# Kernel optimization log

Measured on AMD Instinct MI355X. Metric: run time of the kernel, lower is better.

Reference implementation:

```python
import jax, jax.numpy as jnp
import numpy as np


def setup_inputs() -> dict:
    key = jax.random.key(0)
    ks = jax.random.split(key, 7)
    d, nq, nk = 64, 1024, 2048
    return {
        "query": jax.random.normal(ks[0], (1, d, nq), dtype=jnp.float32),
        "key": jax.random.normal(ks[1], (1, d, nk), dtype=jnp.float32),
        "value": jax.random.normal(ks[2], (1, d, nk), dtype=jnp.float32),
        # Conv1d(2d->d, k=1) weight squeezed to [d, 2d]; Conv1d(d->1, k=1) -> [1, d]
        "W1": jax.random.normal(ks[3], (d, 2 * d), dtype=jnp.float32) * (1.0 / np.sqrt(2 * d)),
        "b1": jax.random.normal(ks[4], (d,), dtype=jnp.float32) * 0.01,
        "W2": jax.random.normal(ks[5], (1, d), dtype=jnp.float32) * (1.0 / np.sqrt(d)),
        "b2": jax.random.normal(ks[6], (1,), dtype=jnp.float32) * 0.01,
    }


def reference(query, key, value, W1, b1, W2, b2):
    d = query.shape[1]
    # Split first conv weight into the query-half and key-half of the concat.
    # Conv1d with kernel 1 on cat([q_bcast, k_bcast]) == W1q @ q + W1k @ k (per pair).
    W1q, W1k = W1[:, :d], W1[:, d:]            # [h, d] each (h == d)
    qp = jnp.einsum('hd,bdq->bqh', W1q, query)  # [1, nq, h]
    kp = jnp.einsum('hd,bdk->bkh', W1k, key)    # [1, nk, h]
    # Pairwise hidden activations [1, nq, nk, h]
    h = jax.nn.relu(qp[:, :, None, :] + kp[:, None, :, :] + b1)
    scores = jnp.einsum('oh,bqkh->bqk', W2, h) + b2[0]  # [1, nq, nk]
    prob = jax.nn.softmax(scores, axis=-1)
    out = jnp.einsum('bnm,bdm->bdn', prob, value)        # [1, d, nq]
    return (out, scores)
```

## Files before the change

kernel.cpp:

```cpp
#include <hip/hip_runtime.h>


__global__ __launch_bounds__(256) void k1_proj(
    const float* __restrict__ q, const float* __restrict__ k,
    const float* __restrict__ W1, const float* __restrict__ b1,
    float* __restrict__ qp, float* __restrict__ kp)
{
  __shared__ float tile[256];
  const int t = threadIdx.x;
  const int b = blockIdx.x;
  if (b < 256) {
    const int nb = (b & 15) << 6;
    const int hb = (b >> 4) << 2;
    const int n = nb + (t & 63);
    const int h = hb + (t >> 6);
    const float* wr = W1 + h * 128;
    float acc = b1[h];
#pragma unroll
    for (int d = 0; d < 64; ++d) acc = fmaf(wr[d], q[(d << 10) + n], acc);
    tile[((t & 63) << 2) + (t >> 6)] = acc;
    __syncthreads();
    qp[((nb + (t >> 2)) << 6) + hb + (t & 3)] = tile[t];
  } else {
    const int b2 = b - 256;
    const int mb = (b2 & 31) << 6;
    const int hb = (b2 >> 5) << 2;
    const int m = mb + (t & 63);
    const int h = hb + (t >> 6);
    const float* wr = W1 + h * 128 + 64;
    float acc = 0.f;
#pragma unroll
    for (int d = 0; d < 64; ++d) acc = fmaf(wr[d], k[(d << 11) + m], acc);
    tile[((t & 63) << 2) + (t >> 6)] = acc;
    __syncthreads();
    kp[((mb + (t >> 2)) << 6) + hb + (t & 3)] = tile[t];
  }
}

__global__ __launch_bounds__(256, 2) void k2_scores(
    const float* __restrict__ qp, const float* __restrict__ kp,
    const float* __restrict__ W2, const float* __restrict__ b2p,
    float* __restrict__ scores, float* __restrict__ lpart)
{
  __shared__ float4 lds4[4096];
  const int t = threadIdx.x;
  const int lane = t & 63;
  const int wave = t >> 6;
  const int qt = blockIdx.x >> 2;
  const int ks = blockIdx.x & 3;
  const int q0 = (qt << 3) + (wave << 1);

  const float4* qp4 = (const float4*)(qp + (q0 << 6));
  float4 qa[16], qb[16];
#pragma unroll
  for (int i = 0; i < 16; ++i) { qa[i] = qp4[i]; qb[i] = qp4[16 + i]; }

  const float4* w24 = (const float4*)W2;
  const float b2v = b2p[0];
  const float4* kp4 = (const float4*)kp;
  const int sw = lane & 15;

  float lacc0 = 0.f, lacc1 = 0.f;

  for (int c = 0; c < 2; ++c) {
    const int kb = (ks << 9) + (c << 8);
    if (c) __syncthreads();
#pragma unroll
    for (int i = 0; i < 16; ++i) {
      const int idx = (i << 8) + t;
      const int row = idx >> 4;
      const int c4 = idx & 15;
      lds4[(row << 4) + (c4 ^ (row & 15))] = kp4[((kb + row) << 4) + c4];
    }
    __syncthreads();
    for (int s = 0; s < 4; ++s) {
      const int kl = (s << 6) + lane;
      float4 A0 = {0.f,0.f,0.f,0.f}, A1 = {0.f,0.f,0.f,0.f};
#pragma unroll
      for (int h4 = 0; h4 < 16; ++h4) {
        const float4 kf = lds4[(kl << 4) + (h4 ^ sw)];
        const float4 wv = w24[h4];
        A0.x = fmaf(wv.x, fmaxf(qa[h4].x + kf.x, 0.f), A0.x);
        A0.y = fmaf(wv.y, fmaxf(qa[h4].y + kf.y, 0.f), A0.y);
        A0.z = fmaf(wv.z, fmaxf(qa[h4].z + kf.z, 0.f), A0.z);
        A0.w = fmaf(wv.w, fmaxf(qa[h4].w + kf.w, 0.f), A0.w);
        A1.x = fmaf(wv.x, fmaxf(qb[h4].x + kf.x, 0.f), A1.x);
        A1.y = fmaf(wv.y, fmaxf(qb[h4].y + kf.y, 0.f), A1.y);
        A1.z = fmaf(wv.z, fmaxf(qb[h4].z + kf.z, 0.f), A1.z);
        A1.w = fmaf(wv.w, fmaxf(qb[h4].w + kf.w, 0.f), A1.w);
      }
      const float s0 = A0.x + A0.y + A0.z + A0.w + b2v;
      const float s1 = A1.x + A1.y + A1.z + A1.w + b2v;
      const int kg = kb + kl;
      scores[(q0 << 11) + kg] = s0;
      scores[((q0 + 1) << 11) + kg] = s1;
      lacc0 += __expf(s0);
      lacc1 += __expf(s1);
    }
  }
#pragma unroll
  for (int off = 32; off > 0; off >>= 1) {
    lacc0 += __shfl_xor(lacc0, off);
    lacc1 += __shfl_xor(lacc1, off);
  }
  if (lane == 0) {
    lpart[(ks << 10) + q0] = lacc0;
    lpart[(ks << 10) + q0 + 1] = lacc1;
  }
}

__global__ __launch_bounds__(256, 2) void k3_pv(
    const float* __restrict__ scores, const float* __restrict__ v,
    float* __restrict__ part)
{
  __shared__ float4 pS4[1024];
  __shared__ float4 vtS4[1024];
  float* vtSf = (float*)vtS4;
  const int t = threadIdx.x;
  const int nt = blockIdx.x >> 5;
  const int ms = blockIdx.x & 31;
  const int n0b = nt << 6;
  const int mc4 = ms << 4;

  const float4* s4 = (const float4*)scores;
  const float4* v4 = (const float4*)v;
#pragma unroll
  for (int i = 0; i < 4; ++i) {
    const int idx = (i << 8) + t;
    const int n = idx >> 4, c = idx & 15;
    float4 val = s4[((n0b + n) << 9) + mc4 + c];
    val.x = __expf(val.x); val.y = __expf(val.y);
    val.z = __expf(val.z); val.w = __expf(val.w);
    pS4[(n << 4) + c] = val;
  }
#pragma unroll
  for (int i = 0; i < 4; ++i) {
    const int idx = (i << 8) + t;
    const int dd = idx >> 4, c = idx & 15;
    const float4 val = v4[(dd << 9) + mc4 + c];
    const int co = (((dd >> 2) ^ c) << 2) + (dd & 3);
    vtSf[(c << 8) + co] = val.x;
    vtSf[(c << 8) + 64 + co] = val.y;
    vtSf[(c << 8) + 128 + co] = val.z;
    vtSf[(c << 8) + 192 + co] = val.w;
  }
  __syncthreads();

  const int tn = t >> 3, td = t & 7;
  const int n0l = tn << 1, n1l = n0l + 1;
  float4 acc00 = {0,0,0,0}, acc01 = {0,0,0,0};
  float4 acc10 = {0,0,0,0}, acc11 = {0,0,0,0};

#define PV_STEP(J, AC) {                                       \
    const float4 b0 = vtS4[(m4 << 6) + (J << 4) + c0];         \
    const float4 b1 = vtS4[(m4 << 6) + (J << 4) + (c0 ^ 8)];   \
    acc00.x = fmaf(a0.AC, b0.x, acc00.x);                      \
    acc00.y = fmaf(a0.AC, b0.y, acc00.y);                      \
    acc00.z = fmaf(a0.AC, b0.z, acc00.z);                      \
    acc00.w = fmaf(a0.AC, b0.w, acc00.w);                      \
    acc01.x = fmaf(a0.AC, b1.x, acc01.x);                      \
    acc01.y = fmaf(a0.AC, b1.y, acc01.y);                      \
    acc01.z = fmaf(a0.AC, b1.z, acc01.z);                      \
    acc01.w = fmaf(a0.AC, b1.w, acc01.w);                      \
    acc10.x = fmaf(a1.AC, b0.x, acc10.x);                      \
    acc10.y = fmaf(a1.AC, b0.y, acc10.y);                      \
    acc10.z = fmaf(a1.AC, b0.z, acc10.z);                      \
    acc10.w = fmaf(a1.AC, b0.w, acc10.w);                      \
    acc11.x = fmaf(a1.AC, b1.x, acc11.x);                      \
    acc11.y = fmaf(a1.AC, b1.y, acc11.y);                      \
    acc11.z = fmaf(a1.AC, b1.z, acc11.z);                      \
    acc11.w = fmaf(a1.AC, b1.w, acc11.w);                      \
  }

#pragma unroll
  for (int m4 = 0; m4 < 16; ++m4) {
    const float4 a0 = pS4[(n0l << 4) + m4];
    const float4 a1 = pS4[(n1l << 4) + m4];
    const int c0 = td ^ m4;
    PV_STEP(0, x) PV_STEP(1, y) PV_STEP(2, z) PV_STEP(3, w)
  }
#undef PV_STEP

  float4* part4 = (float4*)part;
  const int pb0 = (ms << 14) + ((n0b + n0l) << 4);
  const int pb1 = (ms << 14) + ((n0b + n1l) << 4);
  part4[pb0 + td] = acc00;
  part4[pb0 + td + 8] = acc01;
  part4[pb1 + td] = acc10;
  part4[pb1 + td + 8] = acc11;
}

__global__ __launch_bounds__(256) void k4_reduce(
    const float* __restrict__ part, const float* __restrict__ lpart,
    float* __restrict__ out)
{
  __shared__ float oS[256];
  const int t = threadIdx.x;
  const int nb = blockIdx.x << 2;
  const int nl = t >> 6, d = t & 63;
  const int n = nb + nl;
  float sum = 0.f;
#pragma unroll
  for (int ms = 0; ms < 32; ++ms)
    sum += part[(ms << 16) + (n << 6) + d];
  const float l = lpart[n] + lpart[1024 + n] + lpart[2048 + n] + lpart[3072 + n];
  oS[(nl << 6) + d] = sum / l;
  __syncthreads();
  const int d2 = t >> 2, n2 = t & 3;
  out[(d2 << 10) + nb + n2] = oS[(n2 << 6) + d2];
}

extern "C" void kernel_launch(void* const* d_in, const int* in_sizes, int n_in,
                              void* d_out, int out_size, void* d_ws, size_t ws_size,
                              hipStream_t stream) {
  const float* query = (const float*)d_in[0];
  const float* key   = (const float*)d_in[1];
  const float* value = (const float*)d_in[2];
  const float* W1    = (const float*)d_in[3];
  const float* b1    = (const float*)d_in[4];
  const float* W2    = (const float*)d_in[5];
  const float* b2    = (const float*)d_in[6];

  float* out    = (float*)d_out;
  float* scores = out + 65536;

  float* ws    = (float*)d_ws;
  float* qp    = ws;
  float* kp    = ws + 65536;
  float* lpart = ws + 196608;
  float* part  = ws + 200704;

  k1_proj<<<768, 256, 0, stream>>>(query, key, W1, b1, qp, kp);
  k2_scores<<<512, 256, 0, stream>>>(qp, kp, W2, b2, scores, lpart);
  k3_pv<<<512, 256, 0, stream>>>(scores, value, part);
  k4_reduce<<<256, 256, 0, stream>>>(part, lpart, out);
}
```

Before: 103.3 us.

## Retile score kernel into 64x64 q-k tiles with 4x4 register blocking

The pairwise score kernel now loads both a 64-row query tile and a 64-row key tile into swizzled LDS and computes a 4x4 register-blocked outer product per thread, instead of keeping two query rows in registers and streaming 512 keys. Each LDS float4 load now feeds many more FMAs, and scores are written as float4. Partial exp-sums are kept per 64-key tile, so the lpart buffer grows to 32 slices and the reduce kernel sums 32 partials. The cost is more grid tiles and LDS traffic for query data.

```diff
diff --git a/kernel.cpp b/kernel.cpp
--- a/kernel.cpp
+++ b/kernel.cpp
@@ -42,71 +42,82 @@
     const float* __restrict__ W2, const float* __restrict__ b2p,
     float* __restrict__ scores, float* __restrict__ lpart)
 {
-  __shared__ float4 lds4[4096];
-  const int t = threadIdx.x;
-  const int lane = t & 63;
-  const int wave = t >> 6;
-  const int qt = blockIdx.x >> 2;
-  const int ks = blockIdx.x & 3;
-  const int q0 = (qt << 3) + (wave << 1);
-
-  const float4* qp4 = (const float4*)(qp + (q0 << 6));
-  float4 qa[16], qb[16];
-#pragma unroll
-  for (int i = 0; i < 16; ++i) { qa[i] = qp4[i]; qb[i] = qp4[16 + i]; }
-
-  const float4* w24 = (const float4*)W2;
+  __shared__ float4 qS[1024];
+  __shared__ float4 kS[1024];
+  __shared__ float4 wS[16];
+  const int t = threadIdx.x;
+  const int qt = blockIdx.x >> 5;
+  const int kt = blockIdx.x & 31;
+  const int q0b = qt << 6, k0b = kt << 6;
+  const float4* qp4 = (const float4*)qp;
+  const float4* kp4 = (const float4*)kp;
+
+#pragma unroll
+  for (int i = 0; i < 4; ++i) {
+    const int idx = (i << 8) + t;
+    const int row = idx >> 4, c = idx & 15;
+    const int cs = c ^ ((row >> 2) & 15);
+    qS[(row << 4) + cs] = qp4[((q0b + row) << 4) + c];
+    kS[(row << 4) + cs] = kp4[((k0b + row) << 4) + c];
+  }
+  if (t < 16) wS[t] = ((const float4*)W2)[t];
+  __syncthreads();
+
+  const int lane = t & 63, wave = t >> 6;
+  const int lq = lane >> 4, lk = lane & 15;
+  const int ql0 = (wave << 4) + (lq << 2);
+  const int kl0 = lk << 2;
+  const int sq = (wave << 2) | lq;
+
+  float4 acc0 = {0,0,0,0}, acc1 = {0,0,0,0};
+  float4 acc2 = {0,0,0,0}, acc3 = {0,0,0,0};
+
+#pragma unroll 4
+  for (int h4 = 0; h4 < 16; ++h4) {
+    const float4 wv = wS[h4];
+    const int qc = h4 ^ sq, kc = h4 ^ lk;
+    const float4 q0f = qS[((ql0 + 0) << 4) + qc];
+    const float4 q1f = qS[((ql0 + 1) << 4) + qc];
+    const float4 q2f = qS[((ql0 + 2) << 4) + qc];
+    const float4 q3f = qS[((ql0 + 3) << 4) + qc];
+    const float4 k0f = kS[((kl0 + 0) << 4) + kc];
+    const float4 k1f = kS[((kl0 + 1) << 4) + kc];
+    const float4 k2f = kS[((kl0 + 2) << 4) + kc];
+    const float4 k3f = kS[((kl0 + 3) << 4) + kc];
+#define HC(C)                                                        \
+    acc0.x = fmaf(wv.C, fmaxf(q0f.C + k0f.C, 0.f), acc0.x);          \
+    acc0.y = fmaf(wv.C, fmaxf(q0f.C + k1f.C, 0.f), acc0.y);          \
+    acc0.z = fmaf(wv.C, fmaxf(q0f.C + k2f.C, 0.f), acc0.z);          \
+    acc0.w = fmaf(wv.C, fmaxf(q0f.C + k3f.C, 0.f), acc0.w);          \
+    acc1.x = fmaf(wv.C, fmaxf(q1f.C + k0f.C, 0.f), acc1.x);          \
+    acc1.y = fmaf(wv.C, fmaxf(q1f.C + k1f.C, 0.f), acc1.y);          \
+    acc1.z = fmaf(wv.C, fmaxf(q1f.C + k2f.C, 0.f), acc1.z);          \
+    acc1.w = fmaf(wv.C, fmaxf(q1f.C + k3f.C, 0.f), acc1.w);          \
+    acc2.x = fmaf(wv.C, fmaxf(q2f.C + k0f.C, 0.f), acc2.x);          \
+    acc2.y = fmaf(wv.C, fmaxf(q2f.C + k1f.C, 0.f), acc2.y);          \
+    acc2.z = fmaf(wv.C, fmaxf(q2f.C + k2f.C, 0.f), acc2.z);          \
+    acc2.w = fmaf(wv.C, fmaxf(q2f.C + k3f.C, 0.f), acc2.w);          \
+    acc3.x = fmaf(wv.C, fmaxf(q3f.C + k0f.C, 0.f), acc3.x);          \
+    acc3.y = fmaf(wv.C, fmaxf(q3f.C + k1f.C, 0.f), acc3.y);          \
+    acc3.z = fmaf(wv.C, fmaxf(q3f.C + k2f.C, 0.f), acc3.z);          \
+    acc3.w = fmaf(wv.C, fmaxf(q3f.C + k3f.C, 0.f), acc3.w);
+    HC(x) HC(y) HC(z) HC(w)
+#undef HC
+  }
+
   const float b2v = b2p[0];
-  const float4* kp4 = (const float4*)kp;
-  const int sw = lane & 15;
-
-  float lacc0 = 0.f, lacc1 = 0.f;
-
-  for (int c = 0; c < 2; ++c) {
-    const int kb = (ks << 9) + (c << 8);
-    if (c) __syncthreads();
-#pragma unroll
-    for (int i = 0; i < 16; ++i) {
-      const int idx = (i << 8) + t;
-      const int row = idx >> 4;
-      const int c4 = idx & 15;
-      lds4[(row << 4) + (c4 ^ (row & 15))] = kp4[((kb + row) << 4) + c4];
-    }
-    __syncthreads();
-    for (int s = 0; s < 4; ++s) {
-      const int kl = (s << 6) + lane;
-      float4 A0 = {0.f,0.f,0.f,0.f}, A1 = {0.f,0.f,0.f,0.f};
-#pragma unroll
-      for (int h4 = 0; h4 < 16; ++h4) {
-        const float4 kf = lds4[(kl << 4) + (h4 ^ sw)];
-        const float4 wv = w24[h4];
-        A0.x = fmaf(wv.x, fmaxf(qa[h4].x + kf.x, 0.f), A0.x);
-        A0.y = fmaf(wv.y, fmaxf(qa[h4].y + kf.y, 0.f), A0.y);
-        A0.z = fmaf(wv.z, fmaxf(qa[h4].z + kf.z, 0.f), A0.z);
-        A0.w = fmaf(wv.w, fmaxf(qa[h4].w + kf.w, 0.f), A0.w);
-        A1.x = fmaf(wv.x, fmaxf(qb[h4].x + kf.x, 0.f), A1.x);
-        A1.y = fmaf(wv.y, fmaxf(qb[h4].y + kf.y, 0.f), A1.y);
-        A1.z = fmaf(wv.z, fmaxf(qb[h4].z + kf.z, 0.f), A1.z);
-        A1.w = fmaf(wv.w, fmaxf(qb[h4].w + kf.w, 0.f), A1.w);
-      }
-      const float s0 = A0.x + A0.y + A0.z + A0.w + b2v;
-      const float s1 = A1.x + A1.y + A1.z + A1.w + b2v;
-      const int kg = kb + kl;
-      scores[(q0 << 11) + kg] = s0;
-      scores[((q0 + 1) << 11) + kg] = s1;
-      lacc0 += __expf(s0);
-      lacc1 += __expf(s1);
-    }
-  }
-#pragma unroll
-  for (int off = 32; off > 0; off >>= 1) {
-    lacc0 += __shfl_xor(lacc0, off);
-    lacc1 += __shfl_xor(lacc1, off);
-  }
-  if (lane == 0) {
-    lpart[(ks << 10) + q0] = lacc0;
-    lpart[(ks << 10) + q0 + 1] = lacc1;
-  }
+  float4* sc4 = (float4*)scores;
+  const int kcol = (k0b >> 2) + lk;
+#define ROW_OUT(I, ACC) {                                            \
+    float4 s = ACC;                                                  \
+    s.x += b2v; s.y += b2v; s.z += b2v; s.w += b2v;                  \
+    sc4[((q0b + ql0 + I) << 9) + kcol] = s;                          \
+    float e = __expf(s.x) + __expf(s.y) + __expf(s.z) + __expf(s.w); \
+    e += __shfl_xor(e, 1); e += __shfl_xor(e, 2);                    \
+    e += __shfl_xor(e, 4); e += __shfl_xor(e, 8);                    \
+    if (lk == 0) lpart[(kt << 10) + q0b + ql0 + I] = e; }
+  ROW_OUT(0, acc0) ROW_OUT(1, acc1) ROW_OUT(2, acc2) ROW_OUT(3, acc3)
+#undef ROW_OUT
 }
 
 __global__ __launch_bounds__(256, 2) void k3_pv(
@@ -203,7 +214,10 @@
 #pragma unroll
   for (int ms = 0; ms < 32; ++ms)
     sum += part[(ms << 16) + (n << 6) + d];
-  const float l = lpart[n] + lpart[1024 + n] + lpart[2048 + n] + lpart[3072 + n];
+  float l = 0.f;
+#pragma unroll
+  for (int kt = 0; kt < 32; ++kt)
+    l += lpart[(kt << 10) + n];
   oS[(nl << 6) + d] = sum / l;
   __syncthreads();
   const int d2 = t >> 2, n2 = t & 3;
@@ -228,7 +242,7 @@
   float* qp    = ws;
   float* kp    = ws + 65536;
   float* lpart = ws + 196608;
-  float* part  = ws + 200704;
+  float* part  = ws + 229376;
 
   k1_proj<<<768, 256, 0, stream>>>(query, key, W1, b1, qp, kp);
   k2_scores<<<512, 256, 0, stream>>>(qp, kp, W2, b2, scores, lpart);
```

Result: faster. 99.92 us (-3.2%).
